# Kernel tuning notes

Measured on AMD Instinct MI355X. Metric: run time of the kernel, lower is better.

Reference implementation:

```python
import jax, jax.numpy as jnp
import numpy as np

EMBED = 1024
HEADS = 16

def setup_inputs() -> dict:
    key = jax.random.key(0)
    k1, k2, k3, k4, k5 = jax.random.split(key, 5)
    x = jax.random.normal(k1, (2, 2048, EMBED), dtype=jnp.float32)
    s = 1.0 / np.sqrt(EMBED)
    W_atten = jax.random.normal(k2, (EMBED, 3 * EMBED), dtype=jnp.float32) * s
    b_atten = jax.random.normal(k3, (3 * EMBED,), dtype=jnp.float32) * 0.01
    W_proj = jax.random.normal(k4, (EMBED, EMBED), dtype=jnp.float32) * s
    b_proj = jax.random.normal(k5, (EMBED,), dtype=jnp.float32) * 0.01
    return {"x": x, "W_atten": W_atten, "b_atten": b_atten, "W_proj": W_proj, "b_proj": b_proj}

def reference(x, W_atten, b_atten, W_proj, b_proj):
    B, T, C = x.shape
    H = HEADS
    hs = C // H
    qkv = x @ W_atten + b_atten  # [B,T,3C]
    # NOTE: original splits as k, q, v (k first)
    k, q, v = jnp.split(qkv, 3, axis=2)
    k = k.reshape(B, T, H, hs).transpose(0, 2, 1, 3)  # [B,H,T,hs]
    q = q.reshape(B, T, H, hs).transpose(0, 2, 1, 3)
    v = v.reshape(B, T, H, hs).transpose(0, 2, 1, 3)
    scores = jnp.einsum('bhqd,bhkd->bhqk', q, k) / jnp.sqrt(jnp.float32(hs))
    causal = jnp.tril(jnp.ones((T, T), dtype=bool))
    scores = jnp.where(causal[None, None, :, :], scores, jnp.float32(-jnp.inf))
    att = jax.nn.softmax(scores, axis=-1)
    out = jnp.einsum('bhqk,bhkd->bhqd', att, v)  # [B,H,T,hs]
    out = out.transpose(0, 2, 1, 3).reshape(B, T, C)
    return out @ W_proj + b_proj
```

## Files before the change

kernel.cpp:

```cpp
#include <hip/hip_runtime.h>

typedef unsigned short u16;
typedef unsigned int u32;
typedef __bf16 bf16;
typedef bf16 bf16x8 __attribute__((ext_vector_type(8)));
typedef float f32x4 __attribute__((ext_vector_type(4)));
typedef u32 u32x4 __attribute__((ext_vector_type(4)));
typedef u16 u16x4 __attribute__((ext_vector_type(4)));

#define EMBED 1024
#define HEADS 16
#define HS 64
#define BATCH 2
#define SEQ 2048
#define M_TOT (BATCH * SEQ)
#define N_QKV (3 * EMBED)
#define KDIM  EMBED

#define CSCALE 0.18033688011112042f
#define MREF (64.0f * CSCALE)

__device__ __forceinline__ u16 f2bf(float f) {
  u32 u = __builtin_bit_cast(u32, f);
  u32 r = u + 0x7fffu + ((u >> 16) & 1u);
  return (u16)(r >> 16);
}
__device__ __forceinline__ float bf2f(u16 h) {
  return __builtin_bit_cast(float, (u32)h << 16);
}
__device__ __forceinline__ bf16x8 frag16(const u16* p) {
  return __builtin_bit_cast(bf16x8, *(const u32x4*)p);
}
__device__ __forceinline__ bf16x8 frag16u(const u32* p) {
  return __builtin_bit_cast(bf16x8, *(const u32x4*)p);
}
__device__ __forceinline__ float cl(float v) {
  return fminf(fmaxf(v, -3.0e4f), 3.0e4f);
}
__device__ __forceinline__ u32 pk2bf(float lo, float hi) {
  const u32 ul = __builtin_bit_cast(u32, lo) + 0x8000u;
  const u32 uh = __builtin_bit_cast(u32, hi) + 0x8000u;
  return (ul >> 16) | (uh & 0xFFFF0000u);
}

typedef __attribute__((address_space(1))) void gvoid;
typedef __attribute__((address_space(3))) void lvoid;
__device__ __forceinline__ void glds16(const u16* g, u16* l) {
  __builtin_amdgcn_global_load_lds((gvoid*)g, (lvoid*)l, 16, 0, 0);
}

__global__ __launch_bounds__(256) void convert_kernel(
    const float* __restrict__ in, u16* __restrict__ out, int n4) {
  const int i = blockIdx.x * 256 + threadIdx.x;
  if (i < n4) {
    f32x4 v = *(const f32x4*)(in + (size_t)i * 4);
    u16x4 pk;
#pragma unroll
    for (int j = 0; j < 4; j++) pk[j] = f2bf(v[j]);
    *(u16x4*)(out + (size_t)i * 4) = pk;
  }
}

__global__ __launch_bounds__(256) void transpose_conv_kernel(
    const float* __restrict__ in, u16* __restrict__ out, int R, int C) {
  __shared__ u16 tile[32][33];
  const int c0 = blockIdx.x * 32;
  const int r0 = blockIdx.y * 32;
  const int tx = threadIdx.x;
  const int ty = threadIdx.y;
#pragma unroll
  for (int i = 0; i < 32; i += 8)
    tile[ty + i][tx] = f2bf(in[(size_t)(r0 + ty + i) * C + c0 + tx]);
  __syncthreads();
#pragma unroll
  for (int i = 0; i < 32; i += 8)
    out[(size_t)(c0 + ty + i) * R + r0 + tx] = tile[tx][ty + i];
}

__global__ __launch_bounds__(256) void gemm_qkv_kernel(
    const u16* __restrict__ A, const u16* __restrict__ wt,
    const u16* __restrict__ bias, u16* __restrict__ kq, u16* __restrict__ vt) {
  __shared__ u16 As[128 * 32];
  __shared__ u16 Bs[128 * 32];
  const int tid = threadIdx.x;
  const int lane = tid & 63;
  const int wave = tid >> 6;
  const int quad = lane >> 4;
  const int l16 = lane & 15;
  const int wr = wave >> 1;
  const int wc = wave & 1;
  const int m0 = blockIdx.y * 128;
  const int n0 = blockIdx.x * 128;

  f32x4 acc[4][4] = {};
  const int grow = tid >> 2;
  const int gcol = (tid & 3) * 8;

  for (int k0 = 0; k0 < KDIM; k0 += 32) {
    __syncthreads();
    glds16(A + (size_t)(m0 + grow) * KDIM + k0 + gcol, As + tid * 8);
    glds16(A + (size_t)(m0 + grow + 64) * KDIM + k0 + gcol, As + 2048 + tid * 8);
    glds16(wt + (size_t)(n0 + grow) * KDIM + k0 + gcol, Bs + tid * 8);
    glds16(wt + (size_t)(n0 + grow + 64) * KDIM + k0 + gcol, Bs + 2048 + tid * 8);
    __syncthreads();

    bf16x8 af[4], bfr[4];
#pragma unroll
    for (int i = 0; i < 4; i++) {
      af[i]  = frag16(As + (wr * 64 + i * 16 + l16) * 32 + quad * 8);
      bfr[i] = frag16(Bs + (wc * 64 + i * 16 + l16) * 32 + quad * 8);
    }
#pragma unroll
    for (int mi = 0; mi < 4; mi++)
#pragma unroll
      for (int ni = 0; ni < 4; ni++)
        acc[mi][ni] = __builtin_amdgcn_mfma_f32_16x16x32_bf16(
            af[mi], bfr[ni], acc[mi][ni], 0, 0, 0);
  }

#pragma unroll
  for (int ni = 0; ni < 4; ni++) {
    const int n = n0 + wc * 64 + ni * 16 + l16;
    const float bv = bf2f(bias[n]);
    if (n < 2 * EMBED) {
#pragma unroll
      for (int mi = 0; mi < 4; mi++)
#pragma unroll
        for (int r = 0; r < 4; r++) {
          const int m = m0 + wr * 64 + mi * 16 + quad * 4 + r;
          kq[(size_t)m * 2048 + n] = f2bf(cl(acc[mi][ni][r] + bv));
        }
    } else {
      const int hd = n - 2 * EMBED;
#pragma unroll
      for (int mi = 0; mi < 4; mi++) {
        const int mbase = m0 + wr * 64 + mi * 16 + quad * 4;
        const int bqi = mbase >> 11;
        const int t0 = mbase & 2047;
        u16x4 pk;
#pragma unroll
        for (int r = 0; r < 4; r++) pk[r] = f2bf(cl(acc[mi][ni][r] + bv));
        *(u16x4*)(vt + ((size_t)bqi * EMBED + hd) * SEQ + t0) = pk;
      }
    }
  }
}

__global__ __launch_bounds__(128) void gemm_proj_kernel(
    const u16* __restrict__ A, const u16* __restrict__ wt,
    const u16* __restrict__ bias, float* __restrict__ out) {
  __shared__ u16 As[128 * 32];
  __shared__ u16 Bs[64 * 32];
  const int tid = threadIdx.x;
  const int lane = tid & 63;
  const int wave = tid >> 6;
  const int quad = lane >> 4;
  const int l16 = lane & 15;
  const int m0 = blockIdx.y * 128;
  const int n0 = blockIdx.x * 64;

  f32x4 acc[4][4] = {};
  const int grow = tid >> 2;
  const int gcol = (tid & 3) * 8;

  for (int k0 = 0; k0 < KDIM; k0 += 32) {
    __syncthreads();
#pragma unroll
    for (int p = 0; p < 4; p++)
      glds16(A + (size_t)(m0 + p * 32 + grow) * KDIM + k0 + gcol,
             As + p * 1024 + tid * 8);
#pragma unroll
    for (int p = 0; p < 2; p++)
      glds16(wt + (size_t)(n0 + p * 32 + grow) * KDIM + k0 + gcol,
             Bs + p * 1024 + tid * 8);
    __syncthreads();

    bf16x8 af[4], bfr[4];
#pragma unroll
    for (int i = 0; i < 4; i++) {
      af[i]  = frag16(As + (wave * 64 + i * 16 + l16) * 32 + quad * 8);
      bfr[i] = frag16(Bs + (i * 16 + l16) * 32 + quad * 8);
    }
#pragma unroll
    for (int mi = 0; mi < 4; mi++)
#pragma unroll
      for (int ni = 0; ni < 4; ni++)
        acc[mi][ni] = __builtin_amdgcn_mfma_f32_16x16x32_bf16(
            af[mi], bfr[ni], acc[mi][ni], 0, 0, 0);
  }

#pragma unroll
  for (int ni = 0; ni < 4; ni++) {
    const int n = n0 + ni * 16 + l16;
    const float bv = bf2f(bias[n]);
#pragma unroll
    for (int mi = 0; mi < 4; mi++)
#pragma unroll
      for (int r = 0; r < 4; r++) {
        const int m = m0 + wave * 64 + mi * 16 + quad * 4 + r;
        out[(size_t)m * EMBED + n] = cl(acc[mi][ni][r] + bv);
      }
  }
}

__global__ __launch_bounds__(64) void attn_kernel(
    const u16* __restrict__ kq, const u16* __restrict__ vt,
    u16* __restrict__ att) {
  __shared__ u16 Ks[2][64 * 64];
  __shared__ u32 Ps32[2][16 * 32];

  const int tid = threadIdx.x;
  const int quad = (tid >> 4) & 3;
  const int l16 = tid & 15;

  const int bh = blockIdx.x;
  const int qt32 = 63 - (int)blockIdx.y;
  const int q0 = qt32 * 32;
  const int bq = bh >> 4;
  const int h = bh & 15;

  int qg[2];
  bf16x8 bq0[2], bq1[2];
#pragma unroll
  for (int g = 0; g < 2; g++) {
    qg[g] = q0 + g * 16 + l16;
    const size_t qrow = (size_t)(bq * SEQ + qg[g]) * 2048 + EMBED + h * HS;
    bq0[g] = frag16(kq + qrow + quad * 8);
    bq1[g] = frag16(kq + qrow + 32 + quad * 8);
  }

  const u16* kb = kq + (size_t)bq * SEQ * 2048 + h * HS;
  const u16* vb = vt + ((size_t)bq * EMBED + h * HS) * SEQ;
  const int psw32 = (l16 & 7) << 2;

  const int sw = quad ^ (l16 & 7);

  float lsum[2] = {0.0f, 0.0f};
  f32x4 o[2][4] = {};

  const int nkt = (qt32 >> 1) + 1;
#pragma unroll
  for (int p = 0; p < 8; p++) {
    const int row = p * 8 + (tid >> 3);
    const int sgc = (tid & 7) ^ (row & 7);
    glds16(kb + (size_t)row * 2048 + sgc * 8, Ks[0] + row * 64 + (tid & 7) * 8);
  }

  for (int kt = 0; kt < nkt; kt++) {
    const int k0 = kt * 64;
    __syncthreads();
    if (kt + 1 < nkt) {
      const int kn = k0 + 64;
      u16* dst = Ks[(kt + 1) & 1];
#pragma unroll
      for (int p = 0; p < 8; p++) {
        const int row = p * 8 + (tid >> 3);
        const int sgc = (tid & 7) ^ (row & 7);
        glds16(kb + (size_t)(kn + row) * 2048 + sgc * 8, dst + row * 64 + (tid & 7) * 8);
      }
    }
    const u16* KsB = Ks[kt & 1];

    bf16x8 va[2][4];
#pragma unroll
    for (int kc = 0; kc < 2; kc++)
#pragma unroll
      for (int dc = 0; dc < 4; dc++)
        va[kc][dc] = frag16(vb + (size_t)(dc * 16 + l16) * SEQ + k0 + kc * 32 + quad * 8);

    f32x4 st[2][4] = {};
    __builtin_amdgcn_s_setprio(1);
#pragma unroll
    for (int sub = 0; sub < 4; sub++) {
      const u16* kr = KsB + (sub * 16 + l16) * 64;
      const bf16x8 ka0 = frag16(kr + sw * 8);
      const bf16x8 ka1 = frag16(kr + (sw ^ 4) * 8);
#pragma unroll
      for (int g = 0; g < 2; g++) {
        st[g][sub] = __builtin_amdgcn_mfma_f32_16x16x32_bf16(
            ka0, bq0[g], st[g][sub], 0, 0, 0);
        st[g][sub] = __builtin_amdgcn_mfma_f32_16x16x32_bf16(
            ka1, bq1[g], st[g][sub], 0, 0, 0);
      }
    }
    __builtin_amdgcn_s_setprio(0);

    const bool diag = (kt == nkt - 1);
#pragma unroll
    for (int g = 0; g < 2; g++) {
      float p[4][4];
      if (diag) {
#pragma unroll
        for (int sub = 0; sub < 4; sub++)
#pragma unroll
          for (int r = 0; r < 4; r++) {
            const int key = k0 + sub * 16 + quad * 4 + r;
            const float e = __builtin_amdgcn_exp2f(st[g][sub][r] * CSCALE - MREF);
            p[sub][r] = (key <= qg[g]) ? e : 0.0f;
            lsum[g] += p[sub][r];
          }
      } else {
#pragma unroll
        for (int sub = 0; sub < 4; sub++)
#pragma unroll
          for (int r = 0; r < 4; r++) {
            p[sub][r] = __builtin_amdgcn_exp2f(st[g][sub][r] * CSCALE - MREF);
            lsum[g] += p[sub][r];
          }
      }
      u32* pw = Ps32[g];
#pragma unroll
      for (int sub = 0; sub < 4; sub++)
#pragma unroll
        for (int rp = 0; rp < 2; rp++)
          pw[l16 * 32 + ((sub * 8 + quad * 2 + rp) ^ psw32)] =
              pk2bf(p[sub][2 * rp], p[sub][2 * rp + 1]);
    }

#pragma unroll
    for (int g = 0; g < 2; g++) {
      u32* pw = Ps32[g];
#pragma unroll
      for (int kc = 0; kc < 2; kc++) {
        bf16x8 pb = frag16u(pw + l16 * 32 + ((kc * 16 + quad * 4) ^ psw32));
        __builtin_amdgcn_s_setprio(1);
#pragma unroll
        for (int dc = 0; dc < 4; dc++)
          o[g][dc] = __builtin_amdgcn_mfma_f32_16x16x32_bf16(
              va[kc][dc], pb, o[g][dc], 0, 0, 0);
        __builtin_amdgcn_s_setprio(0);
      }
    }
  }

#pragma unroll
  for (int g = 0; g < 2; g++) {
    float ls = lsum[g];
    ls += __shfl_xor(ls, 16);
    ls += __shfl_xor(ls, 32);
    const float inv = 1.0f / ls;
    const size_t obase = (size_t)(bq * SEQ + qg[g]) * EMBED + h * HS;
#pragma unroll
    for (int dc = 0; dc < 4; dc++) {
      u16 sv[4];
#pragma unroll
      for (int r = 0; r < 4; r++) sv[r] = f2bf(cl(o[g][dc][r] * inv));
      *(u32*)(att + obase + dc * 16 + quad * 4) = (u32)sv[0] | ((u32)sv[1] << 16);
      *(u32*)(att + obase + dc * 16 + quad * 4 + 2) = (u32)sv[2] | ((u32)sv[3] << 16);
    }
  }
}

extern "C" void kernel_launch(void* const* d_in, const int* in_sizes, int n_in,
                              void* d_out, int out_size, void* d_ws,
                              size_t ws_size, hipStream_t stream) {
  const float* x       = (const float*)d_in[0];
  const float* W_atten = (const float*)d_in[1];
  const float* b_atten = (const float*)d_in[2];
  const float* W_proj  = (const float*)d_in[3];
  const float* b_proj  = (const float*)d_in[4];

  u16* wt_a = (u16*)d_ws;
  u16* wt_p = wt_a + (size_t)N_QKV * EMBED;
  u16* ba   = wt_p + (size_t)EMBED * EMBED;
  u16* bp   = ba + N_QKV;
  u16* xb   = bp + EMBED;
  u16* kq   = xb + (size_t)M_TOT * KDIM;
  u16* vt   = kq + (size_t)M_TOT * 2048;
  u16* attb = xb;

  convert_kernel<<<(M_TOT * KDIM / 4 + 255) / 256, 256, 0, stream>>>(
      x, xb, M_TOT * KDIM / 4);
  convert_kernel<<<(N_QKV / 4 + 255) / 256, 256, 0, stream>>>(b_atten, ba, N_QKV / 4);
  convert_kernel<<<(EMBED / 4 + 255) / 256, 256, 0, stream>>>(b_proj, bp, EMBED / 4);
  transpose_conv_kernel<<<dim3(N_QKV / 32, EMBED / 32), dim3(32, 8), 0, stream>>>(
      W_atten, wt_a, EMBED, N_QKV);
  transpose_conv_kernel<<<dim3(EMBED / 32, EMBED / 32), dim3(32, 8), 0, stream>>>(
      W_proj, wt_p, EMBED, EMBED);
  gemm_qkv_kernel<<<dim3(N_QKV / 128, M_TOT / 128), 256, 0, stream>>>(
      xb, wt_a, ba, kq, vt);
  attn_kernel<<<dim3(BATCH * HEADS, SEQ / 32), 64, 0, stream>>>(kq, vt, attb);
  gemm_proj_kernel<<<dim3(EMBED / 64, M_TOT / 128), 128, 0, stream>>>(
      attb, wt_p, bp, (float*)d_out);
}
```

Before: 201.9 us.

## Load K fragments directly to registers with double-buffered prefetch, drop LDS staging

The attention kernel no longer stages K tiles through shared memory with async global-to-LDS copies and a barrier. Each lane now loads its K MFMA fragments straight from global memory into a register double buffer. The loop is unrolled by two so the current and next buffers swap without copies. This removes LDS traffic and __syncthreads, but adds register pressure and strided global loads (row stride 2048) that are less coalesced than the LDS path.

Measured after the change: 210.0 us. +4.0%, slower.

```diff
diff --git a/kernel.cpp b/kernel.cpp
--- a/kernel.cpp
+++ b/kernel.cpp
@@ -206,7 +206,6 @@
 __global__ __launch_bounds__(64) void attn_kernel(
     const u16* __restrict__ kq, const u16* __restrict__ vt,
     u16* __restrict__ att) {
-  __shared__ u16 Ks[2][64 * 64];
   __shared__ u32 Ps32[2][16 * 32];
 
   const int tid = threadIdx.x;
@@ -233,33 +232,43 @@
   const u16* vb = vt + ((size_t)bq * EMBED + h * HS) * SEQ;
   const int psw32 = (l16 & 7) << 2;
 
-  const int sw = quad ^ (l16 & 7);
-
   float lsum[2] = {0.0f, 0.0f};
   f32x4 o[2][4] = {};
 
   const int nkt = (qt32 >> 1) + 1;
-#pragma unroll
-  for (int p = 0; p < 8; p++) {
-    const int row = p * 8 + (tid >> 3);
-    const int sgc = (tid & 7) ^ (row & 7);
-    glds16(kb + (size_t)row * 2048 + sgc * 8, Ks[0] + row * 64 + (tid & 7) * 8);
-  }
-
-  for (int kt = 0; kt < nkt; kt++) {
+
+  bf16x8 kA[4][2], kB[4][2];
+#pragma unroll
+  for (int sub = 0; sub < 4; sub++) {
+    const u16* kr = kb + (size_t)(sub * 16 + l16) * 2048 + quad * 8;
+    kA[sub][0] = frag16(kr);
+    kA[sub][1] = frag16(kr + 32);
+  }
+
+  auto body = [&](int kt, bf16x8 (&cur)[4][2], bf16x8 (&nxt)[4][2]) {
     const int k0 = kt * 64;
-    __syncthreads();
     if (kt + 1 < nkt) {
-      const int kn = k0 + 64;
-      u16* dst = Ks[(kt + 1) & 1];
-#pragma unroll
-      for (int p = 0; p < 8; p++) {
-        const int row = p * 8 + (tid >> 3);
-        const int sgc = (tid & 7) ^ (row & 7);
-        glds16(kb + (size_t)(kn + row) * 2048 + sgc * 8, dst + row * 64 + (tid & 7) * 8);
-      }
-    }
-    const u16* KsB = Ks[kt & 1];
+#pragma unroll
+      for (int sub = 0; sub < 4; sub++) {
+        const u16* kr = kb + (size_t)(k0 + 64 + sub * 16 + l16) * 2048 + quad * 8;
+        nxt[sub][0] = frag16(kr);
+        nxt[sub][1] = frag16(kr + 32);
+      }
+    }
+
+    f32x4 st[2][4] = {};
+    __builtin_amdgcn_s_setprio(1);
+#pragma unroll
+    for (int sub = 0; sub < 4; sub++) {
+#pragma unroll
+      for (int g = 0; g < 2; g++) {
+        st[g][sub] = __builtin_amdgcn_mfma_f32_16x16x32_bf16(
+            cur[sub][0], bq0[g], st[g][sub], 0, 0, 0);
+        st[g][sub] = __builtin_amdgcn_mfma_f32_16x16x32_bf16(
+            cur[sub][1], bq1[g], st[g][sub], 0, 0, 0);
+      }
+    }
+    __builtin_amdgcn_s_setprio(0);
 
     bf16x8 va[2][4];
 #pragma unroll
@@ -267,23 +276,6 @@
 #pragma unroll
       for (int dc = 0; dc < 4; dc++)
         va[kc][dc] = frag16(vb + (size_t)(dc * 16 + l16) * SEQ + k0 + kc * 32 + quad * 8);
-
-    f32x4 st[2][4] = {};
-    __builtin_amdgcn_s_setprio(1);
-#pragma unroll
-    for (int sub = 0; sub < 4; sub++) {
-      const u16* kr = KsB + (sub * 16 + l16) * 64;
-      const bf16x8 ka0 = frag16(kr + sw * 8);
-      const bf16x8 ka1 = frag16(kr + (sw ^ 4) * 8);
-#pragma unroll
-      for (int g = 0; g < 2; g++) {
-        st[g][sub] = __builtin_amdgcn_mfma_f32_16x16x32_bf16(
-            ka0, bq0[g], st[g][sub], 0, 0, 0);
-        st[g][sub] = __builtin_amdgcn_mfma_f32_16x16x32_bf16(
-            ka1, bq1[g], st[g][sub], 0, 0, 0);
-      }
-    }
-    __builtin_amdgcn_s_setprio(0);
 
     const bool diag = (kt == nkt - 1);
 #pragma unroll
@@ -331,6 +323,11 @@
         __builtin_amdgcn_s_setprio(0);
       }
     }
+  };
+
+  for (int kt = 0; kt < nkt; kt += 2) {
+    body(kt, kA, kB);
+    if (kt + 1 < nkt) body(kt + 1, kB, kA);
   }
 
 #pragma unroll
```
